# Optimization experiments

Measured on AMD Instinct MI355X. Metric: run time of the kernel, lower is better.

The kernel has to match this reference:

```python
import jax, jax.numpy as jnp
import numpy as np

NUM_HEADS = 8
BN_EPS = 1e-5


def setup_inputs() -> dict:
    key = jax.random.key(0)
    ks = jax.random.split(key, 8)
    B, Ct, Cs, H, W, E = 8, 256, 128, 32, 32, 256
    s = 0.05  # small init scale to keep softmax logits reasonable
    return {
        "tgt": jax.random.normal(ks[0], (B, Ct, H, W), jnp.float32),
        "src": jax.random.normal(ks[1], (B, Cs, H, W), jnp.float32),
        "kv_w": jax.random.normal(ks[2], (E, Cs), jnp.float32) * s,
        "in_proj_w": jax.random.normal(ks[3], (3 * E, E), jnp.float32) * s,
        "in_proj_b": jnp.zeros((3 * E,), jnp.float32),
        "out_proj_w": jax.random.normal(ks[4], (E, E), jnp.float32) * s,
        "out_proj_b": jnp.zeros((E,), jnp.float32),
        "fuse_w": jax.random.normal(ks[5], (Ct, E), jnp.float32) * s,
        "bn_gamma": jnp.ones((Ct,), jnp.float32),
        "bn_beta": jnp.zeros((Ct,), jnp.float32),
        "bn_mean": jnp.zeros((Ct,), jnp.float32),
        "bn_var": jnp.ones((Ct,), jnp.float32),
    }


def reference(tgt, src, kv_w, in_proj_w, in_proj_b, out_proj_w, out_proj_b,
              fuse_w, bn_gamma, bn_beta, bn_mean, bn_var):
    B, Ct, H, W = tgt.shape
    E = kv_w.shape[0]
    nH = NUM_HEADS
    hd = E // nH

    # q_proj is Identity (C_tgt == embed_dim); flatten spatial to tokens [B, Q, E]
    q_seq = tgt.reshape(B, Ct, H * W).transpose(0, 2, 1)
    # kv_proj: 1x1 conv == channel matmul; then flatten to [B, K, E]
    kv_map = jnp.einsum('bchw,ec->behw', src, kv_w)
    k_seq = kv_map.reshape(B, E, H * W).transpose(0, 2, 1)

    # nn.MultiheadAttention: packed in-projection
    Wq, Wk, Wv = in_proj_w[:E], in_proj_w[E:2 * E], in_proj_w[2 * E:]
    bq, bk, bv = in_proj_b[:E], in_proj_b[E:2 * E], in_proj_b[2 * E:]
    qp = (q_seq @ Wq.T + bq).reshape(B, -1, nH, hd).transpose(0, 2, 1, 3)  # [B,h,Q,d]
    kp = (k_seq @ Wk.T + bk).reshape(B, -1, nH, hd).transpose(0, 2, 1, 3)  # [B,h,K,d]
    vp = (k_seq @ Wv.T + bv).reshape(B, -1, nH, hd).transpose(0, 2, 1, 3)  # [B,h,K,d]

    scores = jnp.einsum('bhqd,bhkd->bhqk', qp, kp) / jnp.sqrt(jnp.float32(hd))
    attn = jax.nn.softmax(scores, axis=-1)  # [B,h,Q,K] (non-flash explicit path)

    ctx = jnp.einsum('bhqk,bhkd->bhqd', attn, vp)
    ctx = ctx.transpose(0, 2, 1, 3).reshape(B, -1, E)  # [B,Q,E]
    out_seq = ctx @ out_proj_w.T + out_proj_b

    # cached spatial key-attention map: mean over heads and queries -> [B,1,Hk,Wk]
    attn_map = attn.mean(axis=(1, 2)).reshape(B, 1, H, W)

    # back to map, fuse: 1x1 conv -> BN(eval) -> SiLU, then residual add
    out_map = out_seq.transpose(0, 2, 1).reshape(B, E, H, W)
    fused = jnp.einsum('behw,ce->bchw', out_map, fuse_w)
    inv = bn_gamma / jnp.sqrt(bn_var + BN_EPS)
    bn = (fused - bn_mean[None, :, None, None]) * inv[None, :, None, None] \
         + bn_beta[None, :, None, None]
    y = tgt + bn * jax.nn.sigmoid(bn)  # SiLU
    return y, attn_map
```

## Files before the change

kernel.cpp:

```cpp
#include <hip/hip_runtime.h>
#include <hip/hip_bf16.h>

typedef unsigned short u16;
typedef unsigned int u32;
typedef __attribute__((ext_vector_type(8))) short short8;
typedef __attribute__((ext_vector_type(4))) float f32x4;
typedef __attribute__((ext_vector_type(4))) unsigned short u16x4;
typedef __attribute__((ext_vector_type(4))) int i32x4;

static __device__ __forceinline__ u16 f2bf(float x) {
  __hip_bfloat16 b = __float2bfloat16(x);
  return *reinterpret_cast<u16*>(&b);
}
static __device__ __forceinline__ u32 fbits(float x) {
  union { float f; u32 u; } v; v.f = x; return v.u;
}
static __device__ __forceinline__ u32 pk_trunc(float lo, float hi) {
  return __builtin_amdgcn_perm(fbits(hi), fbits(lo), 0x07060302u);
}
static __device__ __forceinline__ void gl2lds16(const u16* g, u16* l) {
  __builtin_amdgcn_global_load_lds(
      (const __attribute__((address_space(1))) void*)g,
      (__attribute__((address_space(3))) void*)l, 16, 0, 0);
}

#define QSCALE2 (0.17677669529663687f * 1.4426950408889634f)

__global__ __launch_bounds__(256) void prep_xpose(
    const float* __restrict__ in_proj_w, const float* __restrict__ in_proj_b,
    const float* __restrict__ kv_w, const float* __restrict__ fuse_w,
    const float* __restrict__ out_proj_w, const float* __restrict__ out_proj_b,
    const float* __restrict__ gamma, const float* __restrict__ beta,
    const float* __restrict__ mean, const float* __restrict__ var,
    const float* __restrict__ tgt, const float* __restrict__ src,
    u16* __restrict__ WqB, u16* __restrict__ WkvB, u16* __restrict__ M2B,
    float* __restrict__ qbias, float2* __restrict__ bnpk,
    u16* __restrict__ tgtT, u16* __restrict__ srcT) {
  if (blockIdx.x < 769) {
    int idx = blockIdx.x * 256 + threadIdx.x;
    if (idx < 65536) {
      WqB[idx] = f2bf(in_proj_w[idx] * QSCALE2);
    } else if (idx < 131072) {
      int i = idx - 65536;
      int m = i >> 7, c = i & 127;
      const float* wrow = in_proj_w + (size_t)(256 + m) * 256;
      float s = 0.f;
      for (int e2 = 0; e2 < 256; ++e2) s += wrow[e2] * kv_w[e2 * 128 + c];
      WkvB[i] = f2bf(s);
    } else if (idx < 196608) {
      int i = idx - 131072;
      int c = i >> 8, e2 = i & 255;
      float s = 0.f;
      for (int e = 0; e < 256; ++e)
        s += fuse_w[c * 256 + e] * out_proj_w[e * 256 + e2];
      M2B[i] = f2bf(s);
    } else if (idx < 196864) {
      int c = idx - 196608;
      float fbv = 0.f;
      for (int e = 0; e < 256; ++e) fbv += fuse_w[c * 256 + e] * out_proj_b[e];
      float inv = gamma[c] * rsqrtf(var[c] + 1e-5f);
      bnpk[c] = make_float2(inv, (fbv - mean[c]) * inv + beta[c]);
      qbias[c] = in_proj_b[c] * QSCALE2;
    }
    return;
  }
  __shared__ u16 tile[64 * 65];
  int i0 = blockIdx.x - 769;
  int b = i0 / 96, rem = i0 % 96;
  int by = rem >> 4, sb = (rem & 15) * 64;
  const float* X;
  u16* XT;
  int C, cb;
  if (by < 4) {
    X = tgt + (size_t)b * 256 * 1024;
    XT = tgtT + (size_t)b * 1024 * 256;
    C = 256;
    cb = by * 64;
  } else {
    X = src + (size_t)b * 128 * 1024;
    XT = srcT + (size_t)b * 1024 * 128;
    C = 128;
    cb = (by - 4) * 64;
  }
  int t = threadIdx.x;
  for (int i = t; i < 4096; i += 256) {
    int c = i >> 6, s = i & 63;
    tile[c * 65 + s] = f2bf(X[(size_t)(cb + c) * 1024 + sb + s]);
  }
  __syncthreads();
  for (int i = t; i < 4096; i += 256) {
    int s = i >> 6, c = i & 63;
    XT[(size_t)(sb + s) * C + cb + c] = tile[c * 65 + s];
  }
}

__global__ __launch_bounds__(256, 4) void qkv_gemm(
    const u16* __restrict__ tgtT, const u16* __restrict__ srcT,
    const u16* __restrict__ WqB, const u16* __restrict__ WkvB,
    const float* __restrict__ qbias, const float* __restrict__ bkv,
    u16* __restrict__ QB, u16* __restrict__ KB, u16* __restrict__ VB) {
  __shared__ __align__(16) u16 Wl[64 * 32];
  __shared__ __align__(16) u16 Xl[128 * 32];
  int b = blockIdx.z, my = blockIdx.y, n0 = blockIdx.x * 128;
  bool isQ = my < 4;
  int m0 = isQ ? my * 64 : (my - 4) * 64;
  int Kd = isQ ? 256 : 128;
  const u16* Wp = isQ ? WqB : WkvB;
  const u16* Xp = isQ ? tgtT + (size_t)b * 1024 * 256
                      : srcT + (size_t)b * 1024 * 128;
  int t = threadIdx.x, wave = t >> 6, lane = t & 63;
  int lq = lane & 15, quad = lane >> 4;
  int srow = t >> 2, sseg = t & 3;
  f32x4 acc[4][2];
#pragma unroll
  for (int mt = 0; mt < 4; ++mt)
#pragma unroll
    for (int nt = 0; nt < 2; ++nt) acc[mt][nt] = (f32x4){0.f, 0.f, 0.f, 0.f};

  for (int k0 = 0; k0 < Kd; k0 += 32) {
    __syncthreads();
    gl2lds16(&Wp[(size_t)(m0 + srow) * Kd + k0 + sseg * 8], &Wl[wave * 512]);
    gl2lds16(&Xp[(size_t)(n0 + srow) * Kd + k0 + sseg * 8], &Xl[wave * 512]);
    gl2lds16(&Xp[(size_t)(n0 + 64 + srow) * Kd + k0 + sseg * 8],
             &Xl[2048 + wave * 512]);
    __syncthreads();
    short8 af[4], bf[2];
#pragma unroll
    for (int mt = 0; mt < 4; ++mt)
      af[mt] = *(const short8*)&Wl[(mt * 16 + lq) * 32 + quad * 8];
#pragma unroll
    for (int nt = 0; nt < 2; ++nt)
      bf[nt] = *(const short8*)&Xl[(wave * 32 + nt * 16 + lq) * 32 + quad * 8];
#pragma unroll
    for (int mt = 0; mt < 4; ++mt)
#pragma unroll
      for (int nt = 0; nt < 2; ++nt)
        acc[mt][nt] = __builtin_amdgcn_mfma_f32_16x16x32_bf16(af[mt], bf[nt],
                                                              acc[mt][nt], 0, 0, 0);
  }
  if (isQ) {
#pragma unroll
    for (int mt = 0; mt < 4; ++mt) {
      int e = m0 + mt * 16 + quad * 4;
      f32x4 bi = *(const f32x4*)&qbias[e];
#pragma unroll
      for (int nt = 0; nt < 2; ++nt) {
        int n = n0 + wave * 32 + nt * 16 + lq;
        u16x4 pk;
#pragma unroll
        for (int r = 0; r < 4; ++r) pk[r] = f2bf(acc[mt][nt][r] + bi[r]);
        *(u16x4*)&QB[((size_t)b * 1024 + n) * 256 + e] = pk;
      }
    }
  } else {
#pragma unroll
    for (int mt = 0; mt < 4; ++mt) {
      int m = m0 + mt * 16 + quad * 4;
      f32x4 bi = *(const f32x4*)&bkv[m];
#pragma unroll
      for (int nt = 0; nt < 2; ++nt) {
        int n = n0 + wave * 32 + nt * 16 + lq;
        if (m < 256) {
          int hh = m >> 5, d = m & 31;
          u16x4 pk;
#pragma unroll
          for (int r = 0; r < 4; ++r) pk[r] = f2bf(acc[mt][nt][r] + bi[r]);
          *(u16x4*)&KB[((size_t)(b * 8 + hh) * 1024 + n) * 32 + d] = pk;
        } else {
          int e = m - 256;
#pragma unroll
          for (int r = 0; r < 4; ++r)
            VB[((size_t)b * 256 + e + r) * 1024 + n] = f2bf(acc[mt][nt][r] + bi[r]);
        }
      }
    }
  }
}

__global__ __launch_bounds__(256, 4) void attn_passA(
    const u16* __restrict__ QB, const u16* __restrict__ KB,
    const u16* __restrict__ VB, u16* __restrict__ ctxB,
    float* __restrict__ linv_ws) {
  __shared__ __align__(16) u16 Klds[128 * 32];
  __shared__ __align__(16) u16 Vlds[8 * 544];
  int b = blockIdx.z, h = blockIdx.y, q0 = blockIdx.x * 64;
  int t = threadIdx.x, wave = t >> 6, lane = t & 63;
  int lq = lane & 15, quad = lane >> 4;
  int srow = t >> 2, sseg = t & 3;

  const u16* Qb = QB + (size_t)b * 1024 * 256 + h * 32;
  const u16* Kb = KB + (size_t)(b * 8 + h) * 1024 * 32;
  const u16* Vb = VB + (size_t)(b * 256 + h * 32) * 1024;

  int myq = q0 + wave * 16 + lq;
  short8 qf = *(const short8*)(Qb + (size_t)myq * 256 + quad * 8);

  const f32x4 zf = (f32x4){0.f, 0.f, 0.f, 0.f};
  f32x4 O0 = zf, O1 = zf;
  float lsum = 0.f;
  int keyA = ((lq >> 2) << 3) | (lq & 3);

  for (int c0 = 0; c0 < 1024; c0 += 128) {
    __syncthreads();
    gl2lds16(Kb + (size_t)(c0 + srow) * 32 + sseg * 8, &Klds[wave * 512]);
    gl2lds16(Kb + (size_t)(c0 + 64 + srow) * 32 + sseg * 8, &Klds[2048 + wave * 512]);
#pragma unroll
    for (int c = 0; c < 2; ++c) {
      int g = c * 4 + wave;
      int d = g * 4 + (lane >> 4);
      gl2lds16(Vb + (size_t)d * 1024 + c0 + (lane & 15) * 8, &Vlds[g * 544]);
    }
    __syncthreads();
#pragma unroll
    for (int pair = 0; pair < 4; ++pair) {
      short8 kf0 = *(const short8*)&Klds[(pair * 32 + keyA) * 32 + quad * 8];
      short8 kf1 = *(const short8*)&Klds[(pair * 32 + keyA + 4) * 32 + quad * 8];
      f32x4 s0 = __builtin_amdgcn_mfma_f32_16x16x32_bf16(kf0, qf, zf, 0, 0, 0);
      f32x4 s1 = __builtin_amdgcn_mfma_f32_16x16x32_bf16(kf1, qf, zf, 0, 0, 0);
      f32x4 e0, e1;
#pragma unroll
      for (int r = 0; r < 4; ++r) {
        e0[r] = exp2f(s0[r]);
        e1[r] = exp2f(s1[r]);
      }
      lsum += (e0[0] + e0[1]) + (e0[2] + e0[3]) +
              (e1[0] + e1[1]) + (e1[2] + e1[3]);
      i32x4 pi;
      pi[0] = (int)pk_trunc(e0[0], e0[1]);
      pi[1] = (int)pk_trunc(e0[2], e0[3]);
      pi[2] = (int)pk_trunc(e1[0], e1[1]);
      pi[3] = (int)pk_trunc(e1[2], e1[3]);
      short8 pf = *(short8*)&pi;
      short8 vf0 = *(const short8*)&Vlds[((lq >> 2) * 544) + (lq & 3) * 128 +
                                         pair * 32 + quad * 8];
      short8 vf1 = *(const short8*)&Vlds[((4 + (lq >> 2)) * 544) + (lq & 3) * 128 +
                                         pair * 32 + quad * 8];
      O0 = __builtin_amdgcn_mfma_f32_16x16x32_bf16(vf0, pf, O0, 0, 0, 0);
      O1 = __builtin_amdgcn_mfma_f32_16x16x32_bf16(vf1, pf, O1, 0, 0, 0);
    }
  }

  lsum += __shfl_xor(lsum, 16);
  lsum += __shfl_xor(lsum, 32);
  float linv = 1.f / lsum;

  u16x4 pk0, pk1;
#pragma unroll
  for (int r = 0; r < 4; ++r) {
    pk0[r] = f2bf(O0[r] * linv);
    pk1[r] = f2bf(O1[r] * linv);
  }
  u16* crow = ctxB + ((size_t)b * 1024 + myq) * 256 + h * 32 + quad * 4;
  *(u16x4*)crow = pk0;
  *(u16x4*)(crow + 16) = pk1;
  if (quad == 0) linv_ws[(size_t)(b * 8 + h) * 1024 + myq] = linv;
}

__global__ __launch_bounds__(256, 4) void colsum_kernel(
    const u16* __restrict__ QB, const u16* __restrict__ KB,
    const float* __restrict__ linv_ws, float* __restrict__ attn_out) {
  __shared__ __align__(16) u16 Klds[128 * 32];
  __shared__ float colsum[1024];
  int b = blockIdx.z, h = blockIdx.y, q0 = blockIdx.x * 128;
  int t = threadIdx.x, wave = t >> 6, lane = t & 63;
  int lq = lane & 15, quad = lane >> 4;
  int srow = t >> 2, sseg = t & 3;

  const u16* Qb = QB + (size_t)b * 1024 * 256 + h * 32;
  const u16* Kb = KB + (size_t)(b * 8 + h) * 1024 * 32;
  const float* lvp = linv_ws + (size_t)(b * 8 + h) * 1024 + q0 + wave * 32;

  short8 qf2[2];
  f32x4 lv[2];
#pragma unroll
  for (int mt = 0; mt < 2; ++mt) {
    qf2[mt] = *(const short8*)(Qb + (size_t)(q0 + wave * 32 + mt * 16 + lq) * 256 + quad * 8);
    lv[mt] = *(const f32x4*)&lvp[mt * 16 + quad * 4];
  }
  for (int i = t; i < 1024; i += 256) colsum[i] = 0.f;
  const f32x4 zf = (f32x4){0.f, 0.f, 0.f, 0.f};

  for (int c0 = 0; c0 < 1024; c0 += 128) {
    __syncthreads();
    gl2lds16(Kb + (size_t)(c0 + srow) * 32 + sseg * 8, &Klds[wave * 512]);
    gl2lds16(Kb + (size_t)(c0 + 64 + srow) * 32 + sseg * 8, &Klds[2048 + wave * 512]);
    __syncthreads();
#pragma unroll
    for (int nt = 0; nt < 8; ++nt) {
      short8 kf = *(const short8*)&Klds[(nt * 16 + lq) * 32 + quad * 8];
      float cs = 0.f;
#pragma unroll
      for (int mt = 0; mt < 2; ++mt) {
        f32x4 s = __builtin_amdgcn_mfma_f32_16x16x32_bf16(qf2[mt], kf, zf, 0, 0, 0);
        cs += exp2f(s[0]) * lv[mt][0] + exp2f(s[1]) * lv[mt][1] +
              exp2f(s[2]) * lv[mt][2] + exp2f(s[3]) * lv[mt][3];
      }
      cs += __shfl_xor(cs, 16);
      cs += __shfl_xor(cs, 32);
      if (quad == 0) atomicAdd(&colsum[c0 + nt * 16 + lq], cs);
    }
  }
  __syncthreads();
  for (int i = t; i < 1024; i += 256)
    atomicAdd(&attn_out[b * 1024 + i], colsum[i] * (1.f / 8192.f));
}

__global__ __launch_bounds__(256, 4) void fused_out(
    const u16* __restrict__ M2B, const u16* __restrict__ ctxB,
    const float* __restrict__ tgt, const float2* __restrict__ bnpk,
    float* __restrict__ y) {
  __shared__ __align__(16) u16 Al[64 * 32];
  __shared__ __align__(16) u16 Bl[64 * 32];
  int b = blockIdx.z, c0 = blockIdx.y * 64, s0 = blockIdx.x * 64;
  int t = threadIdx.x, wave = t >> 6, lane = t & 63;
  int lq = lane & 15, quad = lane >> 4;
  int srow = t >> 2, sseg = t & 3;
  f32x4 acc[4];
#pragma unroll
  for (int mt = 0; mt < 4; ++mt) acc[mt] = (f32x4){0.f, 0.f, 0.f, 0.f};

  for (int k0 = 0; k0 < 256; k0 += 32) {
    __syncthreads();
    gl2lds16(&M2B[(size_t)(c0 + srow) * 256 + k0 + sseg * 8], &Al[wave * 512]);
    gl2lds16(&ctxB[((size_t)b * 1024 + s0 + srow) * 256 + k0 + sseg * 8],
             &Bl[wave * 512]);
    __syncthreads();
    short8 bf = *(const short8*)&Bl[(wave * 16 + lq) * 32 + quad * 8];
    short8 af[4];
#pragma unroll
    for (int mt = 0; mt < 4; ++mt)
      af[mt] = *(const short8*)&Al[(mt * 16 + lq) * 32 + quad * 8];
#pragma unroll
    for (int mt = 0; mt < 4; ++mt)
      acc[mt] = __builtin_amdgcn_mfma_f32_16x16x32_bf16(af[mt], bf, acc[mt], 0, 0, 0);
  }
  int s = s0 + wave * 16 + lq;
#pragma unroll
  for (int mt = 0; mt < 4; ++mt) {
#pragma unroll
    for (int r = 0; r < 4; ++r) {
      int c = c0 + mt * 16 + quad * 4 + r;
      float2 p = bnpk[c];
      float bn = acc[mt][r] * p.x + p.y;
      float sig = 1.f / (1.f + __expf(-bn));
      size_t idx = ((size_t)b * 256 + c) * 1024 + s;
      y[idx] = tgt[idx] + bn * sig;
    }
  }
}

extern "C" void kernel_launch(void* const* d_in, const int* in_sizes, int n_in,
                              void* d_out, int out_size, void* d_ws, size_t ws_size,
                              hipStream_t stream) {
  const float* tgt = (const float*)d_in[0];
  const float* src = (const float*)d_in[1];
  const float* kv_w = (const float*)d_in[2];
  const float* in_proj_w = (const float*)d_in[3];
  const float* in_proj_b = (const float*)d_in[4];
  const float* out_proj_w = (const float*)d_in[5];
  const float* out_proj_b = (const float*)d_in[6];
  const float* fuse_w = (const float*)d_in[7];
  const float* bn_gamma = (const float*)d_in[8];
  const float* bn_beta = (const float*)d_in[9];
  const float* bn_mean = (const float*)d_in[10];
  const float* bn_var = (const float*)d_in[11];

  char* W = (char*)d_ws;
  u16* WqB = (u16*)W;
  u16* WkvB = (u16*)(W + 131072);
  u16* M2B = (u16*)(W + 262144);
  float* qbias = (float*)(W + 393216);
  float2* bnpk = (float2*)(W + 394240);
  u16* tgtT = (u16*)(W + 397312);
  u16* srcT = tgtT + 2097152;
  u16* QB = srcT + 1048576;
  u16* KB = QB + 2097152;
  u16* VB = KB + 2097152;
  u16* ctxB = VB + 2097152;
  float* linv_ws = (float*)(ctxB + 2097152);

  float* y = (float*)d_out;
  float* attn_out = y + 2097152;

  hipMemsetAsync(attn_out, 0, 8192 * sizeof(float), stream);
  prep_xpose<<<1537, 256, 0, stream>>>(in_proj_w, in_proj_b, kv_w, fuse_w,
                                       out_proj_w, out_proj_b, bn_gamma, bn_beta,
                                       bn_mean, bn_var, tgt, src,
                                       WqB, WkvB, M2B, qbias, bnpk, tgtT, srcT);
  qkv_gemm<<<dim3(8, 12, 8), 256, 0, stream>>>(tgtT, srcT, WqB, WkvB, qbias,
                                               in_proj_b + 256, QB, KB, VB);
  attn_passA<<<dim3(16, 8, 8), 256, 0, stream>>>(QB, KB, VB, ctxB, linv_ws);
  colsum_kernel<<<dim3(8, 8, 8), 256, 0, stream>>>(QB, KB, linv_ws, attn_out);
  fused_out<<<dim3(16, 4, 8), 256, 0, stream>>>(M2B, ctxB, tgt, bnpk, y);
}
```

Baseline: 168.0 us.

## Fuse attention and column-sum kernels, fold memset into prep, deepen GEMM K-steps

```diff
diff --git a/kernel.cpp b/kernel.cpp
--- a/kernel.cpp
+++ b/kernel.cpp
@@ -35,7 +35,13 @@
     const float* __restrict__ tgt, const float* __restrict__ src,
     u16* __restrict__ WqB, u16* __restrict__ WkvB, u16* __restrict__ M2B,
     float* __restrict__ qbias, float2* __restrict__ bnpk,
-    u16* __restrict__ tgtT, u16* __restrict__ srcT) {
+    u16* __restrict__ tgtT, u16* __restrict__ srcT,
+    float* __restrict__ attn_out) {
+  if (blockIdx.x >= 1537) {
+    int i = (blockIdx.x - 1537) * 256 + threadIdx.x;
+    attn_out[i] = 0.f;
+    return;
+  }
   if (blockIdx.x < 769) {
     int idx = blockIdx.x * 256 + threadIdx.x;
     if (idx < 65536) {
@@ -99,8 +105,8 @@
     const u16* __restrict__ WqB, const u16* __restrict__ WkvB,
     const float* __restrict__ qbias, const float* __restrict__ bkv,
     u16* __restrict__ QB, u16* __restrict__ KB, u16* __restrict__ VB) {
-  __shared__ __align__(16) u16 Wl[64 * 32];
-  __shared__ __align__(16) u16 Xl[128 * 32];
+  __shared__ __align__(16) u16 Wl[2][64 * 32];
+  __shared__ __align__(16) u16 Xl[2][128 * 32];
   int b = blockIdx.z, my = blockIdx.y, n0 = blockIdx.x * 128;
   bool isQ = my < 4;
   int m0 = isQ ? my * 64 : (my - 4) * 64;
@@ -117,26 +123,34 @@
 #pragma unroll
     for (int nt = 0; nt < 2; ++nt) acc[mt][nt] = (f32x4){0.f, 0.f, 0.f, 0.f};
 
-  for (int k0 = 0; k0 < Kd; k0 += 32) {
-    __syncthreads();
-    gl2lds16(&Wp[(size_t)(m0 + srow) * Kd + k0 + sseg * 8], &Wl[wave * 512]);
-    gl2lds16(&Xp[(size_t)(n0 + srow) * Kd + k0 + sseg * 8], &Xl[wave * 512]);
-    gl2lds16(&Xp[(size_t)(n0 + 64 + srow) * Kd + k0 + sseg * 8],
-             &Xl[2048 + wave * 512]);
-    __syncthreads();
-    short8 af[4], bf[2];
-#pragma unroll
-    for (int mt = 0; mt < 4; ++mt)
-      af[mt] = *(const short8*)&Wl[(mt * 16 + lq) * 32 + quad * 8];
-#pragma unroll
-    for (int nt = 0; nt < 2; ++nt)
-      bf[nt] = *(const short8*)&Xl[(wave * 32 + nt * 16 + lq) * 32 + quad * 8];
-#pragma unroll
-    for (int mt = 0; mt < 4; ++mt)
+  for (int k0 = 0; k0 < Kd; k0 += 64) {
+    __syncthreads();
+#pragma unroll
+    for (int hh = 0; hh < 2; ++hh) {
+      gl2lds16(&Wp[(size_t)(m0 + srow) * Kd + k0 + hh * 32 + sseg * 8],
+               &Wl[hh][wave * 512]);
+      gl2lds16(&Xp[(size_t)(n0 + srow) * Kd + k0 + hh * 32 + sseg * 8],
+               &Xl[hh][wave * 512]);
+      gl2lds16(&Xp[(size_t)(n0 + 64 + srow) * Kd + k0 + hh * 32 + sseg * 8],
+               &Xl[hh][2048 + wave * 512]);
+    }
+    __syncthreads();
+#pragma unroll
+    for (int hh = 0; hh < 2; ++hh) {
+      short8 af[4], bf[2];
+#pragma unroll
+      for (int mt = 0; mt < 4; ++mt)
+        af[mt] = *(const short8*)&Wl[hh][(mt * 16 + lq) * 32 + quad * 8];
 #pragma unroll
       for (int nt = 0; nt < 2; ++nt)
-        acc[mt][nt] = __builtin_amdgcn_mfma_f32_16x16x32_bf16(af[mt], bf[nt],
-                                                              acc[mt][nt], 0, 0, 0);
+        bf[nt] = *(const short8*)&Xl[hh][(wave * 32 + nt * 16 + lq) * 32 + quad * 8];
+#pragma unroll
+      for (int mt = 0; mt < 4; ++mt)
+#pragma unroll
+        for (int nt = 0; nt < 2; ++nt)
+          acc[mt][nt] = __builtin_amdgcn_mfma_f32_16x16x32_bf16(af[mt], bf[nt],
+                                                                acc[mt][nt], 0, 0, 0);
+    }
   }
   if (isQ) {
 #pragma unroll
@@ -177,129 +191,107 @@
   }
 }
 
-__global__ __launch_bounds__(256, 4) void attn_passA(
+__global__ __launch_bounds__(256, 4) void attn_fused(
     const u16* __restrict__ QB, const u16* __restrict__ KB,
     const u16* __restrict__ VB, u16* __restrict__ ctxB,
-    float* __restrict__ linv_ws) {
-  __shared__ __align__(16) u16 Klds[128 * 32];
-  __shared__ __align__(16) u16 Vlds[8 * 544];
+    float* __restrict__ attn_out) {
+  __shared__ __align__(16) u16 Klds[256 * 32];
+  __shared__ __align__(16) u16 Vlds[2 * 8 * 544];
+  __shared__ float colsum[1024];
   int b = blockIdx.z, h = blockIdx.y, q0 = blockIdx.x * 64;
   int t = threadIdx.x, wave = t >> 6, lane = t & 63;
   int lq = lane & 15, quad = lane >> 4;
-  int srow = t >> 2, sseg = t & 3;
 
   const u16* Qb = QB + (size_t)b * 1024 * 256 + h * 32;
   const u16* Kb = KB + (size_t)(b * 8 + h) * 1024 * 32;
   const u16* Vb = VB + (size_t)(b * 256 + h * 32) * 1024;
 
+  for (int i = t; i < 1024; i += 256) colsum[i] = 0.f;
+
   int myq = q0 + wave * 16 + lq;
   short8 qf = *(const short8*)(Qb + (size_t)myq * 256 + quad * 8);
-
   const f32x4 zf = (f32x4){0.f, 0.f, 0.f, 0.f};
+
+  float lsum = 0.f;
+#pragma unroll 2
+  for (int c = 0; c < 1024; c += 32) {
+    short8 kf0 = *(const short8*)(Kb + (size_t)(c + lq) * 32 + quad * 8);
+    short8 kf1 = *(const short8*)(Kb + (size_t)(c + 16 + lq) * 32 + quad * 8);
+    f32x4 s0 = __builtin_amdgcn_mfma_f32_16x16x32_bf16(kf0, qf, zf, 0, 0, 0);
+    f32x4 s1 = __builtin_amdgcn_mfma_f32_16x16x32_bf16(kf1, qf, zf, 0, 0, 0);
+#pragma unroll
+    for (int r = 0; r < 4; ++r) lsum += exp2f(s0[r]) + exp2f(s1[r]);
+  }
+  lsum += __shfl_xor(lsum, 16);
+  lsum += __shfl_xor(lsum, 32);
+  float linv = 1.f / lsum;
+
+  int keyA = ((lq >> 2) << 3) | (lq & 3);
   f32x4 O0 = zf, O1 = zf;
-  float lsum = 0.f;
-  int keyA = ((lq >> 2) << 3) | (lq & 3);
-
-  for (int c0 = 0; c0 < 1024; c0 += 128) {
-    __syncthreads();
-    gl2lds16(Kb + (size_t)(c0 + srow) * 32 + sseg * 8, &Klds[wave * 512]);
-    gl2lds16(Kb + (size_t)(c0 + 64 + srow) * 32 + sseg * 8, &Klds[2048 + wave * 512]);
-#pragma unroll
-    for (int c = 0; c < 2; ++c) {
-      int g = c * 4 + wave;
-      int d = g * 4 + (lane >> 4);
-      gl2lds16(Vb + (size_t)d * 1024 + c0 + (lane & 15) * 8, &Vlds[g * 544]);
-    }
-    __syncthreads();
-#pragma unroll
-    for (int pair = 0; pair < 4; ++pair) {
+  for (int c0 = 0; c0 < 1024; c0 += 256) {
+    __syncthreads();
+#pragma unroll
+    for (int i = 0; i < 4; ++i) {
+      int cc = wave * 4 + i;
+      gl2lds16(Kb + (size_t)(c0 + cc * 16 + (lane >> 2)) * 32 + (lane & 3) * 8,
+               &Klds[cc * 512]);
+    }
+#pragma unroll
+    for (int i = 0; i < 4; ++i) {
+      int g = wave * 4 + i;
+      int sub = g >> 3, gr = g & 7;
+      int d = gr * 4 + (lane >> 4);
+      gl2lds16(Vb + (size_t)d * 1024 + c0 + sub * 128 + (lane & 15) * 8,
+               &Vlds[sub * 4352 + gr * 544]);
+    }
+    __syncthreads();
+#pragma unroll
+    for (int pair = 0; pair < 8; ++pair) {
       short8 kf0 = *(const short8*)&Klds[(pair * 32 + keyA) * 32 + quad * 8];
       short8 kf1 = *(const short8*)&Klds[(pair * 32 + keyA + 4) * 32 + quad * 8];
       f32x4 s0 = __builtin_amdgcn_mfma_f32_16x16x32_bf16(kf0, qf, zf, 0, 0, 0);
       f32x4 s1 = __builtin_amdgcn_mfma_f32_16x16x32_bf16(kf1, qf, zf, 0, 0, 0);
-      f32x4 e0, e1;
+      float e0[4], e1[4];
 #pragma unroll
       for (int r = 0; r < 4; ++r) {
-        e0[r] = exp2f(s0[r]);
-        e1[r] = exp2f(s1[r]);
+        e0[r] = exp2f(s0[r]) * linv;
+        e1[r] = exp2f(s1[r]) * linv;
       }
-      lsum += (e0[0] + e0[1]) + (e0[2] + e0[3]) +
-              (e1[0] + e1[1]) + (e1[2] + e1[3]);
       i32x4 pi;
       pi[0] = (int)pk_trunc(e0[0], e0[1]);
       pi[1] = (int)pk_trunc(e0[2], e0[3]);
       pi[2] = (int)pk_trunc(e1[0], e1[1]);
       pi[3] = (int)pk_trunc(e1[2], e1[3]);
       short8 pf = *(short8*)&pi;
-      short8 vf0 = *(const short8*)&Vlds[((lq >> 2) * 544) + (lq & 3) * 128 +
-                                         pair * 32 + quad * 8];
-      short8 vf1 = *(const short8*)&Vlds[((4 + (lq >> 2)) * 544) + (lq & 3) * 128 +
-                                         pair * 32 + quad * 8];
+#pragma unroll
+      for (int j = 0; j < 8; ++j) {
+        float v = (j < 4) ? e0[j] : e1[j - 4];
+        v += __shfl_xor(v, 1);
+        v += __shfl_xor(v, 2);
+        v += __shfl_xor(v, 4);
+        v += __shfl_xor(v, 8);
+        if (lq == 0) atomicAdd(&colsum[c0 + pair * 32 + quad * 8 + j], v);
+      }
+      int sub = pair >> 2, p2 = pair & 3;
+      short8 vf0 = *(const short8*)&Vlds[sub * 4352 + (lq >> 2) * 544 +
+                                         (lq & 3) * 128 + p2 * 32 + quad * 8];
+      short8 vf1 = *(const short8*)&Vlds[sub * 4352 + (4 + (lq >> 2)) * 544 +
+                                         (lq & 3) * 128 + p2 * 32 + quad * 8];
       O0 = __builtin_amdgcn_mfma_f32_16x16x32_bf16(vf0, pf, O0, 0, 0, 0);
       O1 = __builtin_amdgcn_mfma_f32_16x16x32_bf16(vf1, pf, O1, 0, 0, 0);
     }
   }
 
-  lsum += __shfl_xor(lsum, 16);
-  lsum += __shfl_xor(lsum, 32);
-  float linv = 1.f / lsum;
-
   u16x4 pk0, pk1;
 #pragma unroll
   for (int r = 0; r < 4; ++r) {
-    pk0[r] = f2bf(O0[r] * linv);
-    pk1[r] = f2bf(O1[r] * linv);
+    pk0[r] = f2bf(O0[r]);
+    pk1[r] = f2bf(O1[r]);
   }
   u16* crow = ctxB + ((size_t)b * 1024 + myq) * 256 + h * 32 + quad * 4;
   *(u16x4*)crow = pk0;
   *(u16x4*)(crow + 16) = pk1;
-  if (quad == 0) linv_ws[(size_t)(b * 8 + h) * 1024 + myq] = linv;
-}
-
-__global__ __launch_bounds__(256, 4) void colsum_kernel(
-    const u16* __restrict__ QB, const u16* __restrict__ KB,
-    const float* __restrict__ linv_ws, float* __restrict__ attn_out) {
-  __shared__ __align__(16) u16 Klds[128 * 32];
-  __shared__ float colsum[1024];
-  int b = blockIdx.z, h = blockIdx.y, q0 = blockIdx.x * 128;
-  int t = threadIdx.x, wave = t >> 6, lane = t & 63;
-  int lq = lane & 15, quad = lane >> 4;
-  int srow = t >> 2, sseg = t & 3;
-
-  const u16* Qb = QB + (size_t)b * 1024 * 256 + h * 32;
-  const u16* Kb = KB + (size_t)(b * 8 + h) * 1024 * 32;
-  const float* lvp = linv_ws + (size_t)(b * 8 + h) * 1024 + q0 + wave * 32;
-
-  short8 qf2[2];
-  f32x4 lv[2];
-#pragma unroll
-  for (int mt = 0; mt < 2; ++mt) {
-    qf2[mt] = *(const short8*)(Qb + (size_t)(q0 + wave * 32 + mt * 16 + lq) * 256 + quad * 8);
-    lv[mt] = *(const f32x4*)&lvp[mt * 16 + quad * 4];
-  }
-  for (int i = t; i < 1024; i += 256) colsum[i] = 0.f;
-  const f32x4 zf = (f32x4){0.f, 0.f, 0.f, 0.f};
-
-  for (int c0 = 0; c0 < 1024; c0 += 128) {
-    __syncthreads();
-    gl2lds16(Kb + (size_t)(c0 + srow) * 32 + sseg * 8, &Klds[wave * 512]);
-    gl2lds16(Kb + (size_t)(c0 + 64 + srow) * 32 + sseg * 8, &Klds[2048 + wave * 512]);
-    __syncthreads();
-#pragma unroll
-    for (int nt = 0; nt < 8; ++nt) {
-      short8 kf = *(const short8*)&Klds[(nt * 16 + lq) * 32 + quad * 8];
-      float cs = 0.f;
-#pragma unroll
-      for (int mt = 0; mt < 2; ++mt) {
-        f32x4 s = __builtin_amdgcn_mfma_f32_16x16x32_bf16(qf2[mt], kf, zf, 0, 0, 0);
-        cs += exp2f(s[0]) * lv[mt][0] + exp2f(s[1]) * lv[mt][1] +
-              exp2f(s[2]) * lv[mt][2] + exp2f(s[3]) * lv[mt][3];
-      }
-      cs += __shfl_xor(cs, 16);
-      cs += __shfl_xor(cs, 32);
-      if (quad == 0) atomicAdd(&colsum[c0 + nt * 16 + lq], cs);
-    }
-  }
+
   __syncthreads();
   for (int i = t; i < 1024; i += 256)
     atomicAdd(&attn_out[b * 1024 + i], colsum[i] * (1.f / 8192.f));
@@ -309,8 +301,8 @@
     const u16* __restrict__ M2B, const u16* __restrict__ ctxB,
     const float* __restrict__ tgt, const float2* __restrict__ bnpk,
     float* __restrict__ y) {
-  __shared__ __align__(16) u16 Al[64 * 32];
-  __shared__ __align__(16) u16 Bl[64 * 32];
+  __shared__ __align__(16) u16 Al[2][64 * 32];
+  __shared__ __align__(16) u16 Bl[2][64 * 32];
   int b = blockIdx.z, c0 = blockIdx.y * 64, s0 = blockIdx.x * 64;
   int t = threadIdx.x, wave = t >> 6, lane = t & 63;
   int lq = lane & 15, quad = lane >> 4;
@@ -319,20 +311,27 @@
 #pragma unroll
   for (int mt = 0; mt < 4; ++mt) acc[mt] = (f32x4){0.f, 0.f, 0.f, 0.f};
 
-  for (int k0 = 0; k0 < 256; k0 += 32) {
-    __syncthreads();
-    gl2lds16(&M2B[(size_t)(c0 + srow) * 256 + k0 + sseg * 8], &Al[wave * 512]);
-    gl2lds16(&ctxB[((size_t)b * 1024 + s0 + srow) * 256 + k0 + sseg * 8],
-             &Bl[wave * 512]);
-    __syncthreads();
-    short8 bf = *(const short8*)&Bl[(wave * 16 + lq) * 32 + quad * 8];
-    short8 af[4];
-#pragma unroll
-    for (int mt = 0; mt < 4; ++mt)
-      af[mt] = *(const short8*)&Al[(mt * 16 + lq) * 32 + quad * 8];
-#pragma unroll
-    for (int mt = 0; mt < 4; ++mt)
-      acc[mt] = __builtin_amdgcn_mfma_f32_16x16x32_bf16(af[mt], bf, acc[mt], 0, 0, 0);
+  for (int k0 = 0; k0 < 256; k0 += 64) {
+    __syncthreads();
+#pragma unroll
+    for (int hh = 0; hh < 2; ++hh) {
+      gl2lds16(&M2B[(size_t)(c0 + srow) * 256 + k0 + hh * 32 + sseg * 8],
+               &Al[hh][wave * 512]);
+      gl2lds16(&ctxB[((size_t)b * 1024 + s0 + srow) * 256 + k0 + hh * 32 + sseg * 8],
+               &Bl[hh][wave * 512]);
+    }
+    __syncthreads();
+#pragma unroll
+    for (int hh = 0; hh < 2; ++hh) {
+      short8 bf = *(const short8*)&Bl[hh][(wave * 16 + lq) * 32 + quad * 8];
+      short8 af[4];
+#pragma unroll
+      for (int mt = 0; mt < 4; ++mt)
+        af[mt] = *(const short8*)&Al[hh][(mt * 16 + lq) * 32 + quad * 8];
+#pragma unroll
+      for (int mt = 0; mt < 4; ++mt)
+        acc[mt] = __builtin_amdgcn_mfma_f32_16x16x32_bf16(af[mt], bf, acc[mt], 0, 0, 0);
+    }
   }
   int s = s0 + wave * 16 + lq;
 #pragma unroll
@@ -377,19 +376,17 @@
   u16* KB = QB + 2097152;
   u16* VB = KB + 2097152;
   u16* ctxB = VB + 2097152;
-  float* linv_ws = (float*)(ctxB + 2097152);
 
   float* y = (float*)d_out;
   float* attn_out = y + 2097152;
 
-  hipMemsetAsync(attn_out, 0, 8192 * sizeof(float), stream);
-  prep_xpose<<<1537, 256, 0, stream>>>(in_proj_w, in_proj_b, kv_w, fuse_w,
+  prep_xpose<<<1569, 256, 0, stream>>>(in_proj_w, in_proj_b, kv_w, fuse_w,
                                        out_proj_w, out_proj_b, bn_gamma, bn_beta,
                                        bn_mean, bn_var, tgt, src,
-                                       WqB, WkvB, M2B, qbias, bnpk, tgtT, srcT);
+                                       WqB, WkvB, M2B, qbias, bnpk, tgtT, srcT,
+                                       attn_out);
   qkv_gemm<<<dim3(8, 12, 8), 256, 0, stream>>>(tgtT, srcT, WqB, WkvB, qbias,
                                                in_proj_b + 256, QB, KB, VB);
-  attn_passA<<<dim3(16, 8, 8), 256, 0, stream>>>(QB, KB, VB, ctxB, linv_ws);
-  colsum_kernel<<<dim3(8, 8, 8), 256, 0, stream>>>(QB, KB, linv_ws, attn_out);
+  attn_fused<<<dim3(16, 8, 8), 256, 0, stream>>>(QB, KB, VB, ctxB, attn_out);
   fused_out<<<dim3(16, 4, 8), 256, 0, stream>>>(M2B, ctxB, tgt, bnpk, y);
 }
```

New measurement: 206.5 us. 22.9% more time.
